# Kernel optimization log

Hardware: AMD Instinct MI355X
Metric: run time of the kernel (lower is better)

## Reference

```python
import jax, jax.numpy as jnp
import numpy as np

B, N, H, E = 32, 256, 128, 16

def setup_inputs() -> dict:
    key = jax.random.key(0)
    k1, k2, k3, k4, k5, k6, k7, k8 = jax.random.split(key, 8)
    h = jax.random.normal(k1, (B, N, H), dtype=jnp.float32)
    edge_attr = jax.random.normal(k2, (B, N, N, E), dtype=jnp.float32)
    adj = jax.random.randint(k3, (B, N, N), 0, 2, dtype=jnp.int32)
    num_nodes = jax.random.randint(k4, (B,), 0, N).astype(jnp.int64)
    # Linear W: in = H + E, out = H (torch convention: y = x @ W.T + b)
    lim_w = 1.0 / np.sqrt(H + E)
    W_w = jax.random.uniform(k5, (H, H + E), jnp.float32, -lim_w, lim_w)
    W_b = jax.random.uniform(k6, (H,), jnp.float32, -lim_w, lim_w)
    lim_u = 1.0 / np.sqrt(H)
    U_w = jax.random.uniform(k7, (H, H), jnp.float32, -lim_u, lim_u)
    U_b = jax.random.uniform(k8, (H,), jnp.float32, -lim_u, lim_u)
    return {"h": h, "edge_attr": edge_attr, "adj": adj, "num_nodes": num_nodes,
            "W_w": W_w, "W_b": W_b, "U_w": U_w, "U_b": U_b}

def reference(h, edge_attr, adj, num_nodes, W_w, W_b, U_w, U_b):
    batch, max_nodes, hidden = h.shape
    # gate[i,j] = 1 if adj[:, i, j].sum() > 0  (condition is over the whole batch,
    # and the message is then added for ALL batch elements — matches the torch loop)
    gate = (adj.sum(axis=0) > 0).astype(h.dtype)            # [N, N]
    # Split W into hidden and edge blocks: W(cat(h_i, e_ij)) = h_i Wh^T + e_ij We^T + b
    Wh = W_w[:, :hidden]                                    # [H, H]
    We = W_w[:, hidden:]                                    # [H, E]
    hW = jnp.einsum('bih,oh->bio', h, Wh)                   # [B, N, H]
    term_h = jnp.einsum('ij,bio->bjo', gate, hW)            # [B, N, H]
    e_sum = jnp.einsum('ij,bije->bje', gate, edge_attr)     # [B, N, E]
    term_e = jnp.einsum('bje,oe->bjo', e_sum, We)           # [B, N, H]
    count = gate.sum(axis=0)                                # [N] — bias added once per active (i,j)
    messages = term_h + term_e + count[None, :, None] * W_b[None, None, :]
    # mask padded nodes
    mask = (jnp.arange(max_nodes)[None, :] < num_nodes[:, None])[..., None]
    messages = messages * mask.astype(h.dtype)
    h_new = jnp.einsum('bnh,oh->bno', h + messages, U_w) + U_b
    return h_new
```

## Files before the change

### kernel.cpp

```cpp
#include <hip/hip_runtime.h>

#define Bn 32
#define Nn 256
#define Hn 128
#define En 16
#define WWC (Hn + En)
#define JT 8
#define IC 8

typedef float v4 __attribute__((ext_vector_type(4)));

__global__ __launch_bounds__(256) void k_stream(const float* __restrict__ edge, const int* __restrict__ adj,
                                                const float* __restrict__ h,
                                                float* __restrict__ epart, float* __restrict__ gate,
                                                float* __restrict__ Ppart) {
    int bid = blockIdx.x, t = threadIdx.x;
    __shared__ v4 sred[128];
    if (bid < 2048) {
        int b = bid >> 6, r = bid & 63, ic = r >> 3, jt = r & 7;
        int ig = t >> 7, vc = t & 127;
        const float* p = edge + ((size_t)b << 20) + (size_t)(ic * 32 + ig) * 4096 + jt * 512 + vc * 4;
        v4 a0 = {0.f,0.f,0.f,0.f}, a1 = a0, a2 = a0, a3 = a0;
        #pragma unroll
        for (int k = 0; k < 16; ++k) {
            v4 v = *reinterpret_cast<const v4*>(p + (size_t)k * 8192);
            if ((k & 3) == 0) a0 += v; else if ((k & 3) == 1) a1 += v;
            else if ((k & 3) == 2) a2 += v; else a3 += v;
        }
        v4 s = (a0 + a1) + (a2 + a3);
        if (ig == 1) sred[vc] = s;
        __syncthreads();
        if (ig == 0) {
            s += sred[vc];
            *reinterpret_cast<v4*>(&epart[((size_t)(ic * 32 + b) * JT + jt) * 512 + vc * 4]) = s;
        }
    } else if (bid < 2304) {
        int i = bid - 2048, j = t;
        int s = 0;
        #pragma unroll
        for (int b = 0; b < Bn; ++b) s += adj[(b * Nn + i) * Nn + j];
        gate[i * Nn + j] = (s > 0) ? 1.0f : 0.0f;
    } else {
        int pb = bid - 2304, b = pb >> 3, ic = pb & 7;
        int hh = t & 127, half = t >> 7;
        float* red = reinterpret_cast<float*>(sred);
        float s = 0.f;
        #pragma unroll
        for (int k = 0; k < 16; ++k)
            s += h[((size_t)b * Nn + ic * 32 + half * 16 + k) * Hn + hh];
        red[t] = s;
        __syncthreads();
        if (t < 128) Ppart[(ic * 32 + b) * Hn + t] = red[t] + red[t + 128];
    }
}

__global__ __launch_bounds__(256) void k_prep(const float* __restrict__ gate, const float* __restrict__ U_w,
                                              const float* __restrict__ W_w, const float* __restrict__ Ppart,
                                              float* __restrict__ count, int* __restrict__ zcnt,
                                              int* __restrict__ zlist, float* __restrict__ U_T,
                                              float* __restrict__ Q) {
    int bid = blockIdx.x, t = threadIdx.x;
    if (bid < Nn) {
        int j = bid;
        bool z = (gate[t * Nn + j] == 0.0f);
        unsigned long long m = __ballot(z);
        int lane = t & 63, w = t >> 6;
        __shared__ int wc[4];
        if (lane == 0) wc[w] = (int)__popcll(m);
        __syncthreads();
        int off = 0;
        for (int q = 0; q < w; ++q) off += wc[q];
        if (z) zlist[j * Nn + off + (int)__popcll(m & ((1ull << lane) - 1ull))] = t;
        if (t == 0) {
            int tot = wc[0] + wc[1] + wc[2] + wc[3];
            zcnt[j] = tot;
            count[j] = (float)(Nn - tot);
        }
    } else if (bid < Nn + 64) {
        int m = (bid - Nn) * 2 + (t >> 7), o = t & 127;
        U_T[m * Hn + o] = U_w[o * Hn + m];
    } else {
        int b = bid - (Nn + 64);
        __shared__ float sP[Hn];
        if (t < 128) {
            float p = 0.f;
            #pragma unroll
            for (int ic = 0; ic < IC; ++ic) p += Ppart[(ic * 32 + b) * Hn + t];
            sP[t] = p;
        }
        __syncthreads();
        if (t < 128) {
            float s = 0.f;
            #pragma unroll 8
            for (int hh = 0; hh < Hn; ++hh) s += W_w[t * WWC + hh] * sP[hh];
            Q[b * Hn + t] = s;
        }
    }
}

__global__ __launch_bounds__(512) void k_final(
    const float* __restrict__ h, const float* __restrict__ U_T, const float* __restrict__ U_b,
    const float* __restrict__ Q, const float* __restrict__ W_w, const float* __restrict__ W_b,
    const float* __restrict__ count, const int* __restrict__ zcnt, const int* __restrict__ zlist,
    const float* __restrict__ epart, const float* __restrict__ edge,
    const int* __restrict__ num_nodes, float* __restrict__ out) {
    int jt = blockIdx.x, j0 = jt * 32, b = blockIdx.y, t = threadIdx.x;
    __shared__ float shj[Hn][33];
    __shared__ float sWe[Hn][17];
    __shared__ float sE[32][17];
    __shared__ float sQ[Hn], sWb[Hn], scnt[32], srbuf[Hn];

    #pragma unroll
    for (int q = 0; q < 2; ++q) {
        int f = t + 512 * q;
        int j = f >> 5, c = f & 31;
        v4 v = *reinterpret_cast<const v4*>(&h[((size_t)b * Nn + j0 + j) * Hn + c * 4]);
        shj[c * 4 + 0][j] = v[0];
        shj[c * 4 + 1][j] = v[1];
        shj[c * 4 + 2][j] = v[2];
        shj[c * 4 + 3][j] = v[3];
    }
    {
        int m = t >> 2, c = t & 3;
        v4 v = *reinterpret_cast<const v4*>(&W_w[m * WWC + Hn + c * 4]);
        sWe[m][c * 4 + 0] = v[0];
        sWe[m][c * 4 + 1] = v[1];
        sWe[m][c * 4 + 2] = v[2];
        sWe[m][c * 4 + 3] = v[3];
    }
    if (t < 128) {
        v4 s = {0.f,0.f,0.f,0.f};
        #pragma unroll
        for (int ic = 0; ic < IC; ++ic)
            s += *reinterpret_cast<const v4*>(&epart[((size_t)(ic * 32 + b) * JT + jt) * 512 + t * 4]);
        int j = t >> 2, e4 = (t & 3) * 4;
        sE[j][e4 + 0] = s[0]; sE[j][e4 + 1] = s[1]; sE[j][e4 + 2] = s[2]; sE[j][e4 + 3] = s[3];
    } else if (t < 256) { sQ[t - 128]  = Q[b * Hn + t - 128]; }
    else if (t < 384)   { sWb[t - 256] = W_b[t - 256]; }
    else if (t < 416)   { scnt[t - 384] = count[j0 + t - 384]; }
    __syncthreads();

    int nn = num_nodes[b];
    for (int jj = 0; jj < 32; ++jj) {
        int zc = zcnt[j0 + jj];
        if (zc > 0) {
            if (t < 128) {
                float r = 0.f;
                for (int z = 0; z < zc; ++z)
                    r += h[((size_t)b * Nn + zlist[(j0 + jj) * Nn + z]) * Hn + t];
                srbuf[t] = r;
            }
            __syncthreads();
            if (t < 128 && (j0 + jj) < nn) {
                float c = 0.f;
                #pragma unroll 8
                for (int hh = 0; hh < Hn; ++hh) c += W_w[t * WWC + hh] * srbuf[hh];
                for (int z = 0; z < zc; ++z) {
                    size_t base = (((size_t)b * Nn + zlist[(j0 + jj) * Nn + z]) * Nn + j0 + jj) * En;
                    for (int e = 0; e < En; ++e) c += sWe[t][e] * edge[base + e];
                }
                shj[t][jj] -= c;
            }
            __syncthreads();
        }
    }

    #pragma unroll
    for (int q = 0; q < 8; ++q) {
        int f = t + 512 * q;
        int m = f >> 5, j = f & 31;
        float y = sQ[m] + scnt[j] * sWb[m];
        #pragma unroll
        for (int e = 0; e < En; ++e) y += sWe[m][e] * sE[j][e];
        if (j0 + j < nn) shj[m][j] += y;
    }
    __syncthreads();

    int og = t & 31, o4 = og * 4, jq = t >> 5, j2 = jq * 2;
    v4 acc0 = {0.f,0.f,0.f,0.f}, acc1 = acc0;
    #pragma unroll 8
    for (int m = 0; m < Hn; ++m) {
        v4 u = *reinterpret_cast<const v4*>(&U_T[m * Hn + o4]);
        acc0 += shj[m][j2] * u;
        acc1 += shj[m][j2 + 1] * u;
    }
    v4 ub = *reinterpret_cast<const v4*>(&U_b[o4]);
    *reinterpret_cast<v4*>(&out[((size_t)b * Nn + j0 + j2) * Hn + o4])     = acc0 + ub;
    *reinterpret_cast<v4*>(&out[((size_t)b * Nn + j0 + j2 + 1) * Hn + o4]) = acc1 + ub;
}

extern "C" void kernel_launch(void* const* d_in, const int* in_sizes, int n_in,
                              void* d_out, int out_size, void* d_ws, size_t ws_size,
                              hipStream_t stream) {
    const float* h    = (const float*)d_in[0];
    const float* edge = (const float*)d_in[1];
    const int*   adj  = (const int*)d_in[2];
    const int*   nn   = (const int*)d_in[3];
    const float* W_w  = (const float*)d_in[4];
    const float* W_b  = (const float*)d_in[5];
    const float* U_w  = (const float*)d_in[6];
    const float* U_b  = (const float*)d_in[7];
    float* out = (float*)d_out;

    float* ws    = (float*)d_ws;
    float* gate  = ws;
    float* count = ws + 65536;
    int*   zcnt  = (int*)(ws + 65792);
    int*   zlist = (int*)(ws + 66048);
    float* Ppart = ws + 131584;
    float* U_T   = ws + 164352;
    float* Q     = ws + 180736;
    float* epart = ws + 184832;

    hipLaunchKernelGGL(k_stream, dim3(2560),      dim3(256), 0, stream, edge, adj, h, epart, gate, Ppart);
    hipLaunchKernelGGL(k_prep,   dim3(352),       dim3(256), 0, stream, gate, U_w, W_w, Ppart,
                       count, zcnt, zlist, U_T, Q);
    hipLaunchKernelGGL(k_final,  dim3(JT, Bn),    dim3(512), 0, stream,
                       h, U_T, U_b, Q, W_w, W_b, count, zcnt, zlist, epart, edge, nn, out);
}
```

Measured before the change: 49.96 us.

## Eliminate prep kernel by folding gate scan, Q and transpose into others

Removes the middle k_prep launch. The U_w transpose moves into the streaming kernel as extra blocks. The per-column zero counts, Q projection and Ppart reduction are now computed inside each final block from a shared-memory copy of the gate tile. The correction path no longer walks a compacted zlist; it scans all 256 rows using the gate mask and pre-sums the edge features into a 16-wide vector before the We product. This saves one launch and a sync point, but every block redundantly recomputes Q and the counts and uses more shared memory, which may lower occupancy.

```diff
diff --git a/kernel.cpp b/kernel.cpp
--- a/kernel.cpp
+++ b/kernel.cpp
@@ -4,16 +4,16 @@
 #define Nn 256
 #define Hn 128
 #define En 16
-#define WWC (Hn + En)
+#define WWC 144
 #define JT 8
 #define IC 8
 
 typedef float v4 __attribute__((ext_vector_type(4)));
 
 __global__ __launch_bounds__(256) void k_stream(const float* __restrict__ edge, const int* __restrict__ adj,
-                                                const float* __restrict__ h,
+                                                const float* __restrict__ h, const float* __restrict__ U_w,
                                                 float* __restrict__ epart, float* __restrict__ gate,
-                                                float* __restrict__ Ppart) {
+                                                float* __restrict__ Ppart, float* __restrict__ U_T) {
     int bid = blockIdx.x, t = threadIdx.x;
     __shared__ v4 sred[128];
     if (bid < 2048) {
@@ -40,7 +40,7 @@
         #pragma unroll
         for (int b = 0; b < Bn; ++b) s += adj[(b * Nn + i) * Nn + j];
         gate[i * Nn + j] = (s > 0) ? 1.0f : 0.0f;
-    } else {
+    } else if (bid < 2560) {
         int pb = bid - 2304, b = pb >> 3, ic = pb & 7;
         int hh = t & 127, half = t >> 7;
         float* red = reinterpret_cast<float*>(sred);
@@ -51,74 +51,39 @@
         red[t] = s;
         __syncthreads();
         if (t < 128) Ppart[(ic * 32 + b) * Hn + t] = red[t] + red[t + 128];
-    }
-}
-
-__global__ __launch_bounds__(256) void k_prep(const float* __restrict__ gate, const float* __restrict__ U_w,
-                                              const float* __restrict__ W_w, const float* __restrict__ Ppart,
-                                              float* __restrict__ count, int* __restrict__ zcnt,
-                                              int* __restrict__ zlist, float* __restrict__ U_T,
-                                              float* __restrict__ Q) {
-    int bid = blockIdx.x, t = threadIdx.x;
-    if (bid < Nn) {
-        int j = bid;
-        bool z = (gate[t * Nn + j] == 0.0f);
-        unsigned long long m = __ballot(z);
-        int lane = t & 63, w = t >> 6;
-        __shared__ int wc[4];
-        if (lane == 0) wc[w] = (int)__popcll(m);
-        __syncthreads();
-        int off = 0;
-        for (int q = 0; q < w; ++q) off += wc[q];
-        if (z) zlist[j * Nn + off + (int)__popcll(m & ((1ull << lane) - 1ull))] = t;
-        if (t == 0) {
-            int tot = wc[0] + wc[1] + wc[2] + wc[3];
-            zcnt[j] = tot;
-            count[j] = (float)(Nn - tot);
-        }
-    } else if (bid < Nn + 64) {
-        int m = (bid - Nn) * 2 + (t >> 7), o = t & 127;
+    } else {
+        int m = (bid - 2560) * 2 + (t >> 7), o = t & 127;
         U_T[m * Hn + o] = U_w[o * Hn + m];
-    } else {
-        int b = bid - (Nn + 64);
-        __shared__ float sP[Hn];
-        if (t < 128) {
-            float p = 0.f;
-            #pragma unroll
-            for (int ic = 0; ic < IC; ++ic) p += Ppart[(ic * 32 + b) * Hn + t];
-            sP[t] = p;
-        }
-        __syncthreads();
-        if (t < 128) {
-            float s = 0.f;
-            #pragma unroll 8
-            for (int hh = 0; hh < Hn; ++hh) s += W_w[t * WWC + hh] * sP[hh];
-            Q[b * Hn + t] = s;
-        }
     }
 }
 
 __global__ __launch_bounds__(512) void k_final(
     const float* __restrict__ h, const float* __restrict__ U_T, const float* __restrict__ U_b,
-    const float* __restrict__ Q, const float* __restrict__ W_w, const float* __restrict__ W_b,
-    const float* __restrict__ count, const int* __restrict__ zcnt, const int* __restrict__ zlist,
-    const float* __restrict__ epart, const float* __restrict__ edge,
+    const float* __restrict__ W_w, const float* __restrict__ W_b, const float* __restrict__ gate,
+    const float* __restrict__ Ppart, const float* __restrict__ epart, const float* __restrict__ edge,
     const int* __restrict__ num_nodes, float* __restrict__ out) {
     int jt = blockIdx.x, j0 = jt * 32, b = blockIdx.y, t = threadIdx.x;
     __shared__ float shj[Hn][33];
+    __shared__ float sgate[Nn][36];
     __shared__ float sWe[Hn][17];
     __shared__ float sE[32][17];
-    __shared__ float sQ[Hn], sWb[Hn], scnt[32], srbuf[Hn];
+    __shared__ float sP[Hn], sQ[Hn], sWb[Hn], srbuf[Hn], sesub[En], scnt[32];
+    __shared__ int szc[32];
 
     #pragma unroll
     for (int q = 0; q < 2; ++q) {
-        int f = t + 512 * q;
-        int j = f >> 5, c = f & 31;
+        int f = t + 512 * q, j = f >> 5, c = f & 31;
         v4 v = *reinterpret_cast<const v4*>(&h[((size_t)b * Nn + j0 + j) * Hn + c * 4]);
         shj[c * 4 + 0][j] = v[0];
         shj[c * 4 + 1][j] = v[1];
         shj[c * 4 + 2][j] = v[2];
         shj[c * 4 + 3][j] = v[3];
+    }
+    #pragma unroll
+    for (int q = 0; q < 4; ++q) {
+        int f = t + 512 * q, i = f >> 3, c = f & 7;
+        *reinterpret_cast<v4*>(&sgate[i][c * 4]) =
+            *reinterpret_cast<const v4*>(&gate[i * Nn + j0 + c * 4]);
     }
     {
         int m = t >> 2, c = t & 3;
@@ -135,30 +100,52 @@
             s += *reinterpret_cast<const v4*>(&epart[((size_t)(ic * 32 + b) * JT + jt) * 512 + t * 4]);
         int j = t >> 2, e4 = (t & 3) * 4;
         sE[j][e4 + 0] = s[0]; sE[j][e4 + 1] = s[1]; sE[j][e4 + 2] = s[2]; sE[j][e4 + 3] = s[3];
-    } else if (t < 256) { sQ[t - 128]  = Q[b * Hn + t - 128]; }
-    else if (t < 384)   { sWb[t - 256] = W_b[t - 256]; }
-    else if (t < 416)   { scnt[t - 384] = count[j0 + t - 384]; }
+    } else if (t < 256) {
+        int hh = t - 128;
+        float p = 0.f;
+        #pragma unroll
+        for (int ic = 0; ic < IC; ++ic) p += Ppart[(ic * 32 + b) * Hn + hh];
+        sP[hh] = p;
+    } else if (t < 384) {
+        sWb[t - 256] = W_b[t - 256];
+    }
+    __syncthreads();
+
+    if (t < 128) {
+        float s = 0.f;
+        #pragma unroll 8
+        for (int hh = 0; hh < Hn; ++hh) s += W_w[t * WWC + hh] * sP[hh];
+        sQ[t] = s;
+    } else if (t < 160) {
+        int jj = t - 128, zc = 0;
+        for (int i = 0; i < Nn; ++i) zc += (sgate[i][jj] == 0.0f) ? 1 : 0;
+        szc[jj] = zc;
+        scnt[jj] = (float)(Nn - zc);
+    }
     __syncthreads();
 
     int nn = num_nodes[b];
     for (int jj = 0; jj < 32; ++jj) {
-        int zc = zcnt[j0 + jj];
-        if (zc > 0) {
+        if (szc[jj] > 0) {
             if (t < 128) {
                 float r = 0.f;
-                for (int z = 0; z < zc; ++z)
-                    r += h[((size_t)b * Nn + zlist[(j0 + jj) * Nn + z]) * Hn + t];
+                for (int i = 0; i < Nn; ++i)
+                    if (sgate[i][jj] == 0.0f) r += h[((size_t)b * Nn + i) * Hn + t];
                 srbuf[t] = r;
+            } else if (t < 144) {
+                int e = t - 128;
+                float r = 0.f;
+                for (int i = 0; i < Nn; ++i)
+                    if (sgate[i][jj] == 0.0f) r += edge[(((size_t)b * Nn + i) * Nn + j0 + jj) * En + e];
+                sesub[e] = r;
             }
             __syncthreads();
             if (t < 128 && (j0 + jj) < nn) {
                 float c = 0.f;
                 #pragma unroll 8
                 for (int hh = 0; hh < Hn; ++hh) c += W_w[t * WWC + hh] * srbuf[hh];
-                for (int z = 0; z < zc; ++z) {
-                    size_t base = (((size_t)b * Nn + zlist[(j0 + jj) * Nn + z]) * Nn + j0 + jj) * En;
-                    for (int e = 0; e < En; ++e) c += sWe[t][e] * edge[base + e];
-                }
+                #pragma unroll
+                for (int e = 0; e < En; ++e) c += sWe[t][e] * sesub[e];
                 shj[t][jj] -= c;
             }
             __syncthreads();
@@ -167,12 +154,13 @@
 
     #pragma unroll
     for (int q = 0; q < 8; ++q) {
-        int f = t + 512 * q;
-        int m = f >> 5, j = f & 31;
-        float y = sQ[m] + scnt[j] * sWb[m];
-        #pragma unroll
-        for (int e = 0; e < En; ++e) y += sWe[m][e] * sE[j][e];
-        if (j0 + j < nn) shj[m][j] += y;
+        int f = t + 512 * q, m = f >> 5, j = f & 31;
+        if (j0 + j < nn) {
+            float y = sQ[m] + scnt[j] * sWb[m];
+            #pragma unroll
+            for (int e = 0; e < En; ++e) y += sWe[m][e] * sE[j][e];
+            shj[m][j] += y;
+        }
     }
     __syncthreads();
 
@@ -204,17 +192,12 @@
 
     float* ws    = (float*)d_ws;
     float* gate  = ws;
-    float* count = ws + 65536;
-    int*   zcnt  = (int*)(ws + 65792);
-    int*   zlist = (int*)(ws + 66048);
-    float* Ppart = ws + 131584;
-    float* U_T   = ws + 164352;
-    float* Q     = ws + 180736;
-    float* epart = ws + 184832;
-
-    hipLaunchKernelGGL(k_stream, dim3(2560),      dim3(256), 0, stream, edge, adj, h, epart, gate, Ppart);
-    hipLaunchKernelGGL(k_prep,   dim3(352),       dim3(256), 0, stream, gate, U_w, W_w, Ppart,
-                       count, zcnt, zlist, U_T, Q);
-    hipLaunchKernelGGL(k_final,  dim3(JT, Bn),    dim3(512), 0, stream,
-                       h, U_T, U_b, Q, W_w, W_b, count, zcnt, zlist, epart, edge, nn, out);
+    float* Ppart = ws + 65536;
+    float* U_T   = ws + 98304;
+    float* epart = ws + 114688;
+
+    hipLaunchKernelGGL(k_stream, dim3(2624),   dim3(256), 0, stream,
+                       edge, adj, h, U_w, epart, gate, Ppart, U_T);
+    hipLaunchKernelGGL(k_final,  dim3(JT, Bn), dim3(512), 0, stream,
+                       h, U_T, U_b, W_w, W_b, gate, Ppart, epart, edge, nn, out);
 }
```

New measurement: 49.02 us. Within noise of the previous version (-1.9%).
